# Kernel tuning notes

Hardware: AMD Instinct MI355X
Metric: run time of the kernel (lower is better)

The kernel has to match this reference:

```python
import jax, jax.numpy as jnp
import numpy as np

ATT_HEADS = 4
H_FEATS = 16
IN_FEATS = 64
N_NODES = 50000
N_EDGES = 1000000


def setup_inputs() -> dict:
    key = jax.random.key(0)
    ks = jax.random.split(key, 12)
    h = jax.random.normal(ks[0], (N_NODES, IN_FEATS), dtype=jnp.float32)
    src_idx = jax.random.randint(ks[1], (N_EDGES,), 0, N_NODES)
    dst_idx = jax.random.randint(ks[2], (N_EDGES,), 0, N_NODES)
    s = 1.0 / np.sqrt(IN_FEATS)
    # w_liner: Linear(in_feats, h_feats*att_heads)
    W_w = jax.random.uniform(ks[3], (IN_FEATS, H_FEATS * ATT_HEADS), jnp.float32, -s, s)
    b_w = jax.random.uniform(ks[4], (H_FEATS * ATT_HEADS,), jnp.float32, -s, s)
    # atten: Linear(2*h_feats, 1)
    sa = 1.0 / np.sqrt(2 * H_FEATS)
    W_a = jax.random.uniform(ks[5], (2 * H_FEATS, 1), jnp.float32, -sa, sa)
    b_a = jax.random.uniform(ks[6], (1,), jnp.float32, -sa, sa)
    # relation_aware: d_liner Linear(in_feats, in_feats), f_liner Linear(3*in_feats, 1)
    W_d = jax.random.uniform(ks[7], (IN_FEATS, IN_FEATS), jnp.float32, -s, s)
    b_d = jax.random.uniform(ks[8], (IN_FEATS,), jnp.float32, -s, s)
    sf = 1.0 / np.sqrt(3 * IN_FEATS)
    W_f = jax.random.uniform(ks[9], (3 * IN_FEATS, 1), jnp.float32, -sf, sf)
    b_f = jax.random.uniform(ks[10], (1,), jnp.float32, -sf, sf)
    return {"h": h, "src_idx": src_idx, "dst_idx": dst_idx,
            "W_w": W_w, "b_w": b_w, "W_a": W_a, "b_a": b_a,
            "W_d": W_d, "b_d": b_d, "W_f": W_f, "b_f": b_f}


def reference(h, src_idx, dst_idx, W_w, b_w, W_a, b_a, W_d, b_d, W_f, b_f):
    N = h.shape[0]
    # sign_edges: relation_aware score -> sign per edge
    s_feat = h[src_idx] @ W_d + b_d            # [E, F]
    d_feat = h[dst_idx] @ W_d + b_d            # [E, F]
    e_feat = jnp.concatenate([s_feat, d_feat, s_feat - d_feat], axis=-1)
    score = jnp.tanh(e_feat @ W_f + b_f)[:, 0]  # [E]
    sign = jnp.sign(score)
    # node transform
    hp = h @ W_w + b_w                          # [N, H*hf]
    # message: signed src features, per-head concat with dst, attention logit
    sf = (sign[:, None] * hp[src_idx]).reshape(-1, ATT_HEADS, H_FEATS)  # [E,H,hf]
    df = hp[dst_idx].reshape(-1, ATT_HEADS, H_FEATS)                    # [E,H,hf]
    z = jnp.concatenate([sf, df], axis=-1)                              # [E,H,2hf]
    alpha = jax.nn.leaky_relu(z @ W_a + b_a)                            # [E,H,1]
    # reduce: segment softmax over incoming edges of each dst node
    amax = jax.ops.segment_max(alpha, dst_idx, num_segments=N)          # [N,H,1]
    ex = jnp.exp(alpha - amax[dst_idx])
    esum = jax.ops.segment_sum(ex, dst_idx, num_segments=N)             # [N,H,1]
    w = ex / esum[dst_idx]                                              # [E,H,1]
    out = jax.ops.segment_sum(w * sf, dst_idx, num_segments=N)          # [N,H,hf]
    return out.reshape(N, ATT_HEADS * H_FEATS)
```

## Files before the change

### kernel.cpp

```cpp
#include <hip/hip_runtime.h>
#include <hip/hip_fp16.h>

constexpr int F  = 64;
constexpr int HEADS = 4;
constexpr int SHARDS = 8;
constexpr int CAPS = 16;
constexpr int MAXDEG = 64;

__global__ __launch_bounds__(256) void node_wd_kernel(
    const float* __restrict__ h,
    const float* __restrict__ W_d, const float* __restrict__ b_d,
    const float* __restrict__ W_f,
    float* __restrict__ tfeat,
    float* __restrict__ u_arr, float* __restrict__ v_arr,
    unsigned* __restrict__ cnt, unsigned* __restrict__ of_cnt, int N)
{
    __shared__ float sWT[F * F];
    __shared__ float sb[F];
    __shared__ double swfA[F], swfB[F];

    int tid = threadIdx.x;
    for (int i = tid; i < F * F; i += 256) {
        int k = i >> 6, j = i & 63;
        sWT[j * F + k] = W_d[i];
    }
    if (tid < F) {
        sb[tid] = b_d[tid];
        swfA[tid] = (double)W_f[tid] + (double)W_f[2 * F + tid];
        swfB[tid] = (double)W_f[F + tid] - (double)W_f[2 * F + tid];
    }
    if (blockIdx.x == 0 && tid == 0) *of_cnt = 0;
    __syncthreads();

    int n = blockIdx.x * 256 + tid;
    if (n >= N) return;

#pragma unroll
    for (int x = 0; x < SHARDS; x++) cnt[(size_t)x * N + n] = 0;

    float4 hv[16];
    const float4* h4 = reinterpret_cast<const float4*>(h + (size_t)n * F);
#pragma unroll
    for (int i = 0; i < 16; i++) hv[i] = h4[i];

    double u = 0.0, v = 0.0;
    float4 tq;
    float4* trow = reinterpret_cast<float4*>(tfeat + (size_t)n * F);
#pragma unroll 4
    for (int j = 0; j < F; j++) {
        const float4* row = reinterpret_cast<const float4*>(&sWT[j * F]);
        float t = 0.f;
#pragma unroll
        for (int kk = 0; kk < 16; kk++) {
            float4 w = row[kk];
            float4 x = hv[kk];
            t = fmaf(x.x, w.x, t);
            t = fmaf(x.y, w.y, t);
            t = fmaf(x.z, w.z, t);
            t = fmaf(x.w, w.w, t);
        }
        t = t + sb[j];
        u = fma((double)t, swfA[j], u);
        v = fma((double)t, swfB[j], v);
        if ((j & 3) == 0) tq.x = t;
        else if ((j & 3) == 1) tq.y = t;
        else if ((j & 3) == 2) tq.z = t;
        else { tq.w = t; trow[j >> 2] = tq; }
    }
    u_arr[n] = (float)u;
    v_arr[n] = (float)v;
}

__device__ __noinline__ float tier2_sign(
    const float* __restrict__ tfeat, const float* __restrict__ sWf,
    int s, int d, float bf)
{
    const float4* ts = reinterpret_cast<const float4*>(tfeat + (size_t)s * F);
    const float4* td = reinterpret_cast<const float4*>(tfeat + (size_t)d * F);
    float sv[F];
#pragma unroll
    for (int i = 0; i < 16; i++) {
        float4 a = ts[i];
        sv[4 * i + 0] = a.x; sv[4 * i + 1] = a.y;
        sv[4 * i + 2] = a.z; sv[4 * i + 3] = a.w;
    }
    float acc = 0.f;
#pragma unroll
    for (int j = 0; j < F; j++) acc = fmaf(sv[j], sWf[j], acc);
#pragma unroll
    for (int i = 0; i < 16; i++) {
        float4 a = td[i];
        acc = fmaf(a.x, sWf[F + 4 * i + 0], acc);
        acc = fmaf(a.y, sWf[F + 4 * i + 1], acc);
        acc = fmaf(a.z, sWf[F + 4 * i + 2], acc);
        acc = fmaf(a.w, sWf[F + 4 * i + 3], acc);
    }
#pragma unroll
    for (int i = 0; i < 16; i++) {
        float4 a = td[i];
        acc = fmaf(sv[4 * i + 0] - a.x, sWf[2 * F + 4 * i + 0], acc);
        acc = fmaf(sv[4 * i + 1] - a.y, sWf[2 * F + 4 * i + 1], acc);
        acc = fmaf(sv[4 * i + 2] - a.z, sWf[2 * F + 4 * i + 2], acc);
        acc = fmaf(sv[4 * i + 3] - a.w, sWf[2 * F + 4 * i + 3], acc);
    }
    float sp = acc + bf;
    return (sp > 0.f) ? 1.f : (sp < 0.f ? -1.f : 0.f);
}

__global__ __launch_bounds__(256) void ww_count_scatter_kernel(
    const float* __restrict__ h,
    const float* __restrict__ W_w, const float* __restrict__ b_w,
    const float* __restrict__ W_a,
    __half* __restrict__ hp,
    float* __restrict__ a_src, float* __restrict__ a_dst,
    const int* __restrict__ src_idx, const int* __restrict__ dst_idx,
    const float* __restrict__ u_arr, const float* __restrict__ v_arr,
    const float* __restrict__ tfeat, const float* __restrict__ W_f,
    const float* __restrict__ b_f,
    unsigned* __restrict__ cnt, unsigned* __restrict__ slot_src,
    unsigned char* __restrict__ sgn8,
    unsigned* __restrict__ of_list, unsigned* __restrict__ of_cnt,
    int N, int E, int nbw, unsigned of_cap)
{
    __shared__ float sWT[F * F];
    __shared__ float sb[F];
    __shared__ float sWa[32];

    int tid = threadIdx.x;

    if (blockIdx.x < nbw) {
        for (int i = tid; i < F * F; i += 256) {
            int k = i >> 6, j = i & 63;
            sWT[j * F + k] = W_w[i];
        }
        if (tid < F) sb[tid] = b_w[tid];
        if (tid < 32) sWa[tid] = W_a[tid];
        __syncthreads();

        int n = blockIdx.x * 256 + tid;
        if (n >= N) return;

        float4 hv[16];
        const float4* h4 = reinterpret_cast<const float4*>(h + (size_t)n * F);
#pragma unroll
        for (int i = 0; i < 16; i++) hv[i] = h4[i];

        __half2* prow = reinterpret_cast<__half2*>(hp + (size_t)n * F);
#pragma unroll
        for (int qh = 0; qh < 4; qh++) {
            float asq = 0.f, adq = 0.f;
            float pprev = 0.f;
#pragma unroll 4
            for (int jj = 0; jj < 16; jj++) {
                int j = qh * 16 + jj;
                const float4* row = reinterpret_cast<const float4*>(&sWT[j * F]);
                float p = 0.f;
#pragma unroll
                for (int kk = 0; kk < 16; kk++) {
                    float4 w = row[kk];
                    float4 x = hv[kk];
                    p = fmaf(x.x, w.x, p);
                    p = fmaf(x.y, w.y, p);
                    p = fmaf(x.z, w.z, p);
                    p = fmaf(x.w, w.w, p);
                }
                p = p + sb[j];
                asq = fmaf(p, sWa[jj], asq);
                adq = fmaf(p, sWa[16 + jj], adq);
                if ((jj & 1) == 0) pprev = p;
                else prow[j >> 1] = __floats2half2_rn(pprev, p);
            }
            a_src[n * HEADS + qh] = asq;
            a_dst[n * HEADS + qh] = adq;
        }
        return;
    }

    float* sWf = sWT;
    if (tid < 3 * F) sWf[tid] = W_f[tid];
    __syncthreads();

    unsigned xcc;
    asm volatile("s_getreg_b32 %0, hwreg(HW_REG_XCC_ID)" : "=s"(xcc));
    xcc &= (SHARDS - 1);

    float bf = b_f[0];
    int eb = blockIdx.x - nbw;
    int e0 = eb * 512 + tid;
    int e1 = e0 + 256;
    bool ok0 = e0 < E, ok1 = e1 < E;

    int s0 = 0, d0 = 0, s1 = 0, d1 = 0;
    if (ok0) { s0 = src_idx[e0]; d0 = dst_idx[e0]; }
    if (ok1) { s1 = src_idx[e1]; d1 = dst_idx[e1]; }

    float us0 = ok0 ? u_arr[s0] : 0.f, vd0 = ok0 ? v_arr[d0] : 0.f;
    float us1 = ok1 ? u_arr[s1] : 0.f, vd1 = ok1 ? v_arr[d1] : 0.f;
    unsigned p0 = ok0 ? __hip_atomic_fetch_add(&cnt[(size_t)xcc * N + d0], 1u,
                          __ATOMIC_RELAXED, __HIP_MEMORY_SCOPE_WORKGROUP) : 0u;
    unsigned p1 = ok1 ? __hip_atomic_fetch_add(&cnt[(size_t)xcc * N + d1], 1u,
                          __ATOMIC_RELAXED, __HIP_MEMORY_SCOPE_WORKGROUP) : 0u;

    bool inl0 = ok0 && (p0 < (unsigned)CAPS);
    bool inl1 = ok1 && (p1 < (unsigned)CAPS);
    size_t idx0 = ((size_t)xcc * N + d0) * CAPS + p0;
    size_t idx1 = ((size_t)xcc * N + d1) * CAPS + p1;
    if (inl0) slot_src[idx0] = (unsigned)s0;
    if (inl1) slot_src[idx1] = (unsigned)s1;

    float m0 = us0 + vd0 + bf;
    float m1 = us1 + vd1 + bf;
    float sg0 = (fabsf(m0) >= 1e-4f) ? ((m0 > 0.f) ? 1.f : -1.f)
              : (ok0 ? tier2_sign(tfeat, sWf, s0, d0, bf) : 0.f);
    float sg1 = (fabsf(m1) >= 1e-4f) ? ((m1 > 0.f) ? 1.f : -1.f)
              : (ok1 ? tier2_sign(tfeat, sWf, s1, d1, bf) : 0.f);
    unsigned c0 = (sg0 > 0.f) ? 0u : (sg0 < 0.f ? 1u : 2u);
    unsigned c1 = (sg1 > 0.f) ? 0u : (sg1 < 0.f ? 1u : 2u);

    if (inl0) sgn8[idx0] = (unsigned char)c0;
    else if (ok0) {
        unsigned oi = atomicAdd(of_cnt, 1u);
        if (oi < of_cap) { of_list[2 * oi] = (unsigned)d0; of_list[2 * oi + 1] = (unsigned)s0 | (c0 << 30); }
    }
    if (inl1) sgn8[idx1] = (unsigned char)c1;
    else if (ok1) {
        unsigned oi = atomicAdd(of_cnt, 1u);
        if (oi < of_cap) { of_list[2 * oi] = (unsigned)d1; of_list[2 * oi + 1] = (unsigned)s1 | (c1 << 30); }
    }
}

__global__ __launch_bounds__(256) void dst_gather_kernel(
    const unsigned* __restrict__ cnt,
    const unsigned* __restrict__ slot_src, const unsigned char* __restrict__ sgn8,
    const unsigned* __restrict__ of_list, const unsigned* __restrict__ of_cnt,
    const float* __restrict__ a_src, const float* __restrict__ a_dst,
    const float* __restrict__ b_a,
    const __half* __restrict__ hp,
    float* __restrict__ out, int N, unsigned of_cap)
{
    __shared__ float sw[4][MAXDEG * 4];
    __shared__ unsigned ssrc[4][MAXDEG];

    int tid = threadIdx.x;
    int wslot = tid >> 6;
    int lane = tid & 63;
    int q = lane >> 4;
    int d = (blockIdx.x * 256 + tid) >> 6;
    bool valid = d < N;

    float ba = b_a[0];
    float4 ad4 = make_float4(0.f, 0.f, 0.f, 0.f);
    unsigned csh[SHARDS], pre[SHARDS];
    unsigned deg = 0;
    bool ofl = false;
    if (valid) {
        ad4 = *reinterpret_cast<const float4*>(a_dst + (size_t)d * HEADS);
#pragma unroll
        for (int x = 0; x < SHARDS; x++) {
            unsigned c = cnt[(size_t)x * N + d];
            csh[x] = c; pre[x] = deg; deg += c;
            if (c > (unsigned)CAPS) ofl = true;
        }
    }
    float adq = (q == 0) ? ad4.x : (q == 1) ? ad4.y : (q == 2) ? ad4.z : ad4.w;
    bool fast = valid && (deg <= (unsigned)MAXDEG) && !ofl;

    float4 p = make_float4(0.f, 0.f, 0.f, 0.f);
    if (fast && lane < (int)deg) {
        int shard = 0; unsigned pos = 0;
#pragma unroll
        for (int x = 0; x < SHARDS; x++)
            if ((unsigned)lane >= pre[x] && (unsigned)lane < pre[x] + csh[x]) {
                shard = x; pos = (unsigned)lane - pre[x];
            }
        size_t idx = ((size_t)shard * N + d) * CAPS + pos;
        unsigned s = slot_src[idx];
        unsigned c = sgn8[idx];
        float sgn = (c == 0u) ? 1.f : (c == 1u ? -1.f : 0.f);
        float4 as4 = *reinterpret_cast<const float4*>(a_src + (size_t)s * HEADS);
        float ap0 = fmaf(sgn, as4.x, ad4.x) + ba;
        float ap1 = fmaf(sgn, as4.y, ad4.y) + ba;
        float ap2 = fmaf(sgn, as4.z, ad4.z) + ba;
        float ap3 = fmaf(sgn, as4.w, ad4.w) + ba;
        float e0 = expf(ap0 > 0.f ? ap0 : 0.01f * ap0);
        float e1 = expf(ap1 > 0.f ? ap1 : 0.01f * ap1);
        float e2 = expf(ap2 > 0.f ? ap2 : 0.01f * ap2);
        float e3 = expf(ap3 > 0.f ? ap3 : 0.01f * ap3);
        p = make_float4(e0, e1, e2, e3);
        *reinterpret_cast<float4*>(&sw[wslot][lane * 4]) =
            make_float4(sgn * e0, sgn * e1, sgn * e2, sgn * e3);
        ssrc[wslot][lane] = s;
    }
    if (valid && !fast) {
        for (int x = 0; x < SHARDS; x++) {
            unsigned cc = min(csh[x], (unsigned)CAPS);
            for (unsigned i = lane; i < cc; i += 64) {
                size_t idx = ((size_t)x * N + d) * CAPS + i;
                unsigned s = slot_src[idx];
                unsigned c = sgn8[idx];
                float sgn = (c == 0u) ? 1.f : (c == 1u ? -1.f : 0.f);
                float4 as4 = *reinterpret_cast<const float4*>(a_src + (size_t)s * HEADS);
                float ap0 = fmaf(sgn, as4.x, ad4.x) + ba;
                float ap1 = fmaf(sgn, as4.y, ad4.y) + ba;
                float ap2 = fmaf(sgn, as4.z, ad4.z) + ba;
                float ap3 = fmaf(sgn, as4.w, ad4.w) + ba;
                p.x += expf(ap0 > 0.f ? ap0 : 0.01f * ap0);
                p.y += expf(ap1 > 0.f ? ap1 : 0.01f * ap1);
                p.z += expf(ap2 > 0.f ? ap2 : 0.01f * ap2);
                p.w += expf(ap3 > 0.f ? ap3 : 0.01f * ap3);
            }
        }
        unsigned on = min(*of_cnt, of_cap);
        for (unsigned i = lane; i < on; i += 64) {
            if (of_list[2 * i] == (unsigned)d) {
                unsigned sp = of_list[2 * i + 1];
                unsigned s = sp & 0x3FFFFFFFu;
                unsigned c = sp >> 30;
                float sgn = (c == 0u) ? 1.f : (c == 1u ? -1.f : 0.f);
                float4 as4 = *reinterpret_cast<const float4*>(a_src + (size_t)s * HEADS);
                float ap0 = fmaf(sgn, as4.x, ad4.x) + ba;
                float ap1 = fmaf(sgn, as4.y, ad4.y) + ba;
                float ap2 = fmaf(sgn, as4.z, ad4.z) + ba;
                float ap3 = fmaf(sgn, as4.w, ad4.w) + ba;
                p.x += expf(ap0 > 0.f ? ap0 : 0.01f * ap0);
                p.y += expf(ap1 > 0.f ? ap1 : 0.01f * ap1);
                p.z += expf(ap2 > 0.f ? ap2 : 0.01f * ap2);
                p.w += expf(ap3 > 0.f ? ap3 : 0.01f * ap3);
            }
        }
    }
    __syncthreads();

#pragma unroll
    for (int off = 32; off >= 1; off >>= 1) {
        p.x += __shfl_xor(p.x, off);
        p.y += __shfl_xor(p.y, off);
        p.z += __shfl_xor(p.z, off);
        p.w += __shfl_xor(p.w, off);
    }
    if (!valid) return;

    float esq = (q == 0) ? p.x : (q == 1) ? p.y : (q == 2) ? p.z : p.w;
    float rinv = (deg > 0) ? (1.0f / esq) : 0.f;

    float a0 = 0.f, a1 = 0.f, a2 = 0.f, a3 = 0.f;
    if (fast) {
        const float* swb = &sw[wslot][0];
        const unsigned* ssb = &ssrc[wslot][0];
        unsigned t0 = 0;
        for (; t0 + 8 <= deg; t0 += 8) {
            float w0 = swb[(t0 + 0) * 4 + q], w1 = swb[(t0 + 1) * 4 + q];
            float w2 = swb[(t0 + 2) * 4 + q], w3 = swb[(t0 + 3) * 4 + q];
            float w4 = swb[(t0 + 4) * 4 + q], w5 = swb[(t0 + 5) * 4 + q];
            float w6 = swb[(t0 + 6) * 4 + q], w7 = swb[(t0 + 7) * 4 + q];
            unsigned s0 = ssb[t0 + 0], s1 = ssb[t0 + 1];
            unsigned s2 = ssb[t0 + 2], s3 = ssb[t0 + 3];
            unsigned s4 = ssb[t0 + 4], s5 = ssb[t0 + 5];
            unsigned s6 = ssb[t0 + 6], s7 = ssb[t0 + 7];
            float h0 = __half2float(hp[((size_t)s0 << 6) | (unsigned)lane]);
            float h1 = __half2float(hp[((size_t)s1 << 6) | (unsigned)lane]);
            float h2 = __half2float(hp[((size_t)s2 << 6) | (unsigned)lane]);
            float h3 = __half2float(hp[((size_t)s3 << 6) | (unsigned)lane]);
            float h4 = __half2float(hp[((size_t)s4 << 6) | (unsigned)lane]);
            float h5 = __half2float(hp[((size_t)s5 << 6) | (unsigned)lane]);
            float h6 = __half2float(hp[((size_t)s6 << 6) | (unsigned)lane]);
            float h7 = __half2float(hp[((size_t)s7 << 6) | (unsigned)lane]);
            a0 = fmaf(w0, h0, a0); a1 = fmaf(w1, h1, a1);
            a2 = fmaf(w2, h2, a2); a3 = fmaf(w3, h3, a3);
            a0 = fmaf(w4, h4, a0); a1 = fmaf(w5, h5, a1);
            a2 = fmaf(w6, h6, a2); a3 = fmaf(w7, h7, a3);
        }
        for (; t0 < deg; t0++) {
            float w = swb[t0 * 4 + q];
            unsigned s = ssb[t0];
            a0 = fmaf(w, __half2float(hp[((size_t)s << 6) | (unsigned)lane]), a0);
        }
    } else {
        for (int x = 0; x < SHARDS; x++) {
            unsigned cc = min(csh[x], (unsigned)CAPS);
            for (unsigned i = 0; i < cc; i++) {
                size_t idx = ((size_t)x * N + d) * CAPS + i;
                unsigned s = slot_src[idx];
                unsigned c = sgn8[idx];
                float g = (c == 0u) ? 1.f : (c == 1u ? -1.f : 0.f);
                float asv = a_src[s * HEADS + q];
                float ap = fmaf(g, asv, adq) + ba;
                float ev = expf(ap > 0.f ? ap : 0.01f * ap);
                a0 = fmaf(ev * g, __half2float(hp[((size_t)s << 6) | (unsigned)lane]), a0);
            }
        }
        unsigned on = min(*of_cnt, of_cap);
        for (unsigned i = 0; i < on; i++) {
            if (of_list[2 * i] == (unsigned)d) {
                unsigned sp = of_list[2 * i + 1];
                unsigned s = sp & 0x3FFFFFFFu;
                unsigned c = sp >> 30;
                float g = (c == 0u) ? 1.f : (c == 1u ? -1.f : 0.f);
                float asv = a_src[s * HEADS + q];
                float ap = fmaf(g, asv, adq) + ba;
                float ev = expf(ap > 0.f ? ap : 0.01f * ap);
                a0 = fmaf(ev * g, __half2float(hp[((size_t)s << 6) | (unsigned)lane]), a0);
            }
        }
    }
    out[((size_t)d << 6) | (unsigned)lane] = ((a0 + a1) + (a2 + a3)) * rinv;
}

extern "C" void kernel_launch(void* const* d_in, const int* in_sizes, int n_in,
                              void* d_out, int out_size, void* d_ws, size_t ws_size,
                              hipStream_t stream)
{
    const float* h       = (const float*)d_in[0];
    const int*   src_idx = (const int*)d_in[1];
    const int*   dst_idx = (const int*)d_in[2];
    const float* W_w     = (const float*)d_in[3];
    const float* b_w     = (const float*)d_in[4];
    const float* W_a     = (const float*)d_in[5];
    const float* b_a     = (const float*)d_in[6];
    const float* W_d     = (const float*)d_in[7];
    const float* b_d     = (const float*)d_in[8];
    const float* W_f     = (const float*)d_in[9];
    const float* b_f     = (const float*)d_in[10];

    int N = in_sizes[0] / F;
    int E = in_sizes[1];
    int nb = (N + 255) / 256;
    int neb = (E + 511) / 512;
    unsigned of_cap = (unsigned)(E / 8);

    char* ws = (char*)d_ws;
    float*         tfeat  = (float*)ws;         ws += (size_t)N * F * 4;
    __half*        hp     = (__half*)ws;        ws += (size_t)N * F * 2;
    float*         u_arr  = (float*)ws;         ws += (size_t)N * 4;
    float*         v_arr  = (float*)ws;         ws += (size_t)N * 4;
    float*         a_src  = (float*)ws;         ws += (size_t)N * HEADS * 4;
    float*         a_dst  = (float*)ws;         ws += (size_t)N * HEADS * 4;
    unsigned*      cnt    = (unsigned*)ws;      ws += (size_t)SHARDS * N * 4;
    unsigned*      of_cnt = (unsigned*)ws;      ws += 64;
    unsigned*      slot_s = (unsigned*)ws;      ws += (size_t)SHARDS * N * CAPS * 4;
    unsigned char* sgn8   = (unsigned char*)ws; ws += (size_t)SHARDS * N * CAPS;
    unsigned*      of_list= (unsigned*)ws;      ws += (size_t)of_cap * 8;

    float* out = (float*)d_out;

    node_wd_kernel<<<nb, 256, 0, stream>>>(
        h, W_d, b_d, W_f, tfeat, u_arr, v_arr, cnt, of_cnt, N);

    ww_count_scatter_kernel<<<nb + neb, 256, 0, stream>>>(
        h, W_w, b_w, W_a, hp, a_src, a_dst,
        src_idx, dst_idx, u_arr, v_arr, tfeat, W_f, b_f,
        cnt, slot_s, sgn8, of_list, of_cnt, N, E, nb, of_cap);

    dst_gather_kernel<<<(N * 64 + 255) / 256, 256, 0, stream>>>(
        cnt, slot_s, sgn8, of_list, of_cnt, a_src, a_dst, b_a, hp, out, N, of_cap);
}
```

Before: 128.0 us.

## Add per-node overflow bucket and halve per-shard slot capacity

```diff
diff --git a/kernel.cpp b/kernel.cpp
--- a/kernel.cpp
+++ b/kernel.cpp
@@ -4,7 +4,8 @@
 constexpr int F  = 64;
 constexpr int HEADS = 4;
 constexpr int SHARDS = 8;
-constexpr int CAPS = 16;
+constexpr int CAPS = 8;
+constexpr int OCAP = 56;
 constexpr int MAXDEG = 64;
 
 __global__ __launch_bounds__(256) void node_wd_kernel(
@@ -13,7 +14,8 @@
     const float* __restrict__ W_f,
     float* __restrict__ tfeat,
     float* __restrict__ u_arr, float* __restrict__ v_arr,
-    unsigned* __restrict__ cnt, unsigned* __restrict__ of_cnt, int N)
+    unsigned* __restrict__ cnt, unsigned* __restrict__ ocnt,
+    unsigned* __restrict__ of_cnt, int N)
 {
     __shared__ float sWT[F * F];
     __shared__ float sb[F];
@@ -37,6 +39,7 @@
 
 #pragma unroll
     for (int x = 0; x < SHARDS; x++) cnt[(size_t)x * N + n] = 0;
+    ocnt[n] = 0;
 
     float4 hv[16];
     const float4* h4 = reinterpret_cast<const float4*>(h + (size_t)n * F);
@@ -119,6 +122,7 @@
     const float* __restrict__ b_f,
     unsigned* __restrict__ cnt, unsigned* __restrict__ slot_src,
     unsigned char* __restrict__ sgn8,
+    unsigned* __restrict__ ocnt, unsigned* __restrict__ ovf,
     unsigned* __restrict__ of_list, unsigned* __restrict__ of_cnt,
     int N, int E, int nbw, unsigned of_cap)
 {
@@ -219,19 +223,28 @@
 
     if (inl0) sgn8[idx0] = (unsigned char)c0;
     else if (ok0) {
-        unsigned oi = atomicAdd(of_cnt, 1u);
-        if (oi < of_cap) { of_list[2 * oi] = (unsigned)d0; of_list[2 * oi + 1] = (unsigned)s0 | (c0 << 30); }
+        unsigned po = atomicAdd(&ocnt[d0], 1u);
+        if (po < (unsigned)OCAP) ovf[(size_t)d0 * OCAP + po] = (unsigned)s0 | (c0 << 30);
+        else {
+            unsigned oi = atomicAdd(of_cnt, 1u);
+            if (oi < of_cap) { of_list[2 * oi] = (unsigned)d0; of_list[2 * oi + 1] = (unsigned)s0 | (c0 << 30); }
+        }
     }
     if (inl1) sgn8[idx1] = (unsigned char)c1;
     else if (ok1) {
-        unsigned oi = atomicAdd(of_cnt, 1u);
-        if (oi < of_cap) { of_list[2 * oi] = (unsigned)d1; of_list[2 * oi + 1] = (unsigned)s1 | (c1 << 30); }
+        unsigned po = atomicAdd(&ocnt[d1], 1u);
+        if (po < (unsigned)OCAP) ovf[(size_t)d1 * OCAP + po] = (unsigned)s1 | (c1 << 30);
+        else {
+            unsigned oi = atomicAdd(of_cnt, 1u);
+            if (oi < of_cap) { of_list[2 * oi] = (unsigned)d1; of_list[2 * oi + 1] = (unsigned)s1 | (c1 << 30); }
+        }
     }
 }
 
 __global__ __launch_bounds__(256) void dst_gather_kernel(
     const unsigned* __restrict__ cnt,
     const unsigned* __restrict__ slot_src, const unsigned char* __restrict__ sgn8,
+    const unsigned* __restrict__ ocnt, const unsigned* __restrict__ ovf,
     const unsigned* __restrict__ of_list, const unsigned* __restrict__ of_cnt,
     const float* __restrict__ a_src, const float* __restrict__ a_dst,
     const float* __restrict__ b_a,
@@ -251,31 +264,41 @@
     float ba = b_a[0];
     float4 ad4 = make_float4(0.f, 0.f, 0.f, 0.f);
     unsigned csh[SHARDS], pre[SHARDS];
-    unsigned deg = 0;
-    bool ofl = false;
+    unsigned degS = 0, oc = 0, ocr = 0;
     if (valid) {
         ad4 = *reinterpret_cast<const float4*>(a_dst + (size_t)d * HEADS);
 #pragma unroll
         for (int x = 0; x < SHARDS; x++) {
             unsigned c = cnt[(size_t)x * N + d];
-            csh[x] = c; pre[x] = deg; deg += c;
-            if (c > (unsigned)CAPS) ofl = true;
-        }
+            csh[x] = min(c, (unsigned)CAPS);
+            pre[x] = degS;
+            degS += csh[x];
+        }
+        ocr = ocnt[d];
+        oc = min(ocr, (unsigned)OCAP);
     }
     float adq = (q == 0) ? ad4.x : (q == 1) ? ad4.y : (q == 2) ? ad4.z : ad4.w;
-    bool fast = valid && (deg <= (unsigned)MAXDEG) && !ofl;
+    unsigned degT = degS + oc;
+    bool fast = valid && (degT <= (unsigned)MAXDEG) && (ocr <= (unsigned)OCAP);
 
     float4 p = make_float4(0.f, 0.f, 0.f, 0.f);
-    if (fast && lane < (int)deg) {
-        int shard = 0; unsigned pos = 0;
-#pragma unroll
-        for (int x = 0; x < SHARDS; x++)
-            if ((unsigned)lane >= pre[x] && (unsigned)lane < pre[x] + csh[x]) {
-                shard = x; pos = (unsigned)lane - pre[x];
-            }
-        size_t idx = ((size_t)shard * N + d) * CAPS + pos;
-        unsigned s = slot_src[idx];
-        unsigned c = sgn8[idx];
+    if (fast && lane < (int)degT) {
+        unsigned s, c;
+        if ((unsigned)lane < degS) {
+            int shard = 0; unsigned pos = 0;
+#pragma unroll
+            for (int x = 0; x < SHARDS; x++)
+                if ((unsigned)lane >= pre[x] && (unsigned)lane < pre[x] + csh[x]) {
+                    shard = x; pos = (unsigned)lane - pre[x];
+                }
+            size_t idx = ((size_t)shard * N + d) * CAPS + pos;
+            s = slot_src[idx];
+            c = sgn8[idx];
+        } else {
+            unsigned v = ovf[(size_t)d * OCAP + ((unsigned)lane - degS)];
+            s = v & 0x3FFFFFFFu;
+            c = v >> 30;
+        }
         float sgn = (c == 0u) ? 1.f : (c == 1u ? -1.f : 0.f);
         float4 as4 = *reinterpret_cast<const float4*>(a_src + (size_t)s * HEADS);
         float ap0 = fmaf(sgn, as4.x, ad4.x) + ba;
@@ -293,8 +316,7 @@
     }
     if (valid && !fast) {
         for (int x = 0; x < SHARDS; x++) {
-            unsigned cc = min(csh[x], (unsigned)CAPS);
-            for (unsigned i = lane; i < cc; i += 64) {
+            for (unsigned i = lane; i < csh[x]; i += 64) {
                 size_t idx = ((size_t)x * N + d) * CAPS + i;
                 unsigned s = slot_src[idx];
                 unsigned c = sgn8[idx];
@@ -309,6 +331,21 @@
                 p.z += expf(ap2 > 0.f ? ap2 : 0.01f * ap2);
                 p.w += expf(ap3 > 0.f ? ap3 : 0.01f * ap3);
             }
+        }
+        for (unsigned i = lane; i < oc; i += 64) {
+            unsigned v = ovf[(size_t)d * OCAP + i];
+            unsigned s = v & 0x3FFFFFFFu;
+            unsigned c = v >> 30;
+            float sgn = (c == 0u) ? 1.f : (c == 1u ? -1.f : 0.f);
+            float4 as4 = *reinterpret_cast<const float4*>(a_src + (size_t)s * HEADS);
+            float ap0 = fmaf(sgn, as4.x, ad4.x) + ba;
+            float ap1 = fmaf(sgn, as4.y, ad4.y) + ba;
+            float ap2 = fmaf(sgn, as4.z, ad4.z) + ba;
+            float ap3 = fmaf(sgn, as4.w, ad4.w) + ba;
+            p.x += expf(ap0 > 0.f ? ap0 : 0.01f * ap0);
+            p.y += expf(ap1 > 0.f ? ap1 : 0.01f * ap1);
+            p.z += expf(ap2 > 0.f ? ap2 : 0.01f * ap2);
+            p.w += expf(ap3 > 0.f ? ap3 : 0.01f * ap3);
         }
         unsigned on = min(*of_cnt, of_cap);
         for (unsigned i = lane; i < on; i += 64) {
@@ -341,14 +378,14 @@
     if (!valid) return;
 
     float esq = (q == 0) ? p.x : (q == 1) ? p.y : (q == 2) ? p.z : p.w;
-    float rinv = (deg > 0) ? (1.0f / esq) : 0.f;
+    float rinv = (esq > 0.f) ? (1.0f / esq) : 0.f;
 
     float a0 = 0.f, a1 = 0.f, a2 = 0.f, a3 = 0.f;
     if (fast) {
         const float* swb = &sw[wslot][0];
         const unsigned* ssb = &ssrc[wslot][0];
         unsigned t0 = 0;
-        for (; t0 + 8 <= deg; t0 += 8) {
+        for (; t0 + 8 <= degT; t0 += 8) {
             float w0 = swb[(t0 + 0) * 4 + q], w1 = swb[(t0 + 1) * 4 + q];
             float w2 = swb[(t0 + 2) * 4 + q], w3 = swb[(t0 + 3) * 4 + q];
             float w4 = swb[(t0 + 4) * 4 + q], w5 = swb[(t0 + 5) * 4 + q];
@@ -370,15 +407,14 @@
             a0 = fmaf(w4, h4, a0); a1 = fmaf(w5, h5, a1);
             a2 = fmaf(w6, h6, a2); a3 = fmaf(w7, h7, a3);
         }
-        for (; t0 < deg; t0++) {
+        for (; t0 < degT; t0++) {
             float w = swb[t0 * 4 + q];
             unsigned s = ssb[t0];
             a0 = fmaf(w, __half2float(hp[((size_t)s << 6) | (unsigned)lane]), a0);
         }
     } else {
         for (int x = 0; x < SHARDS; x++) {
-            unsigned cc = min(csh[x], (unsigned)CAPS);
-            for (unsigned i = 0; i < cc; i++) {
+            for (unsigned i = 0; i < csh[x]; i++) {
                 size_t idx = ((size_t)x * N + d) * CAPS + i;
                 unsigned s = slot_src[idx];
                 unsigned c = sgn8[idx];
@@ -388,6 +424,16 @@
                 float ev = expf(ap > 0.f ? ap : 0.01f * ap);
                 a0 = fmaf(ev * g, __half2float(hp[((size_t)s << 6) | (unsigned)lane]), a0);
             }
+        }
+        for (unsigned i = 0; i < oc; i++) {
+            unsigned v = ovf[(size_t)d * OCAP + i];
+            unsigned s = v & 0x3FFFFFFFu;
+            unsigned c = v >> 30;
+            float g = (c == 0u) ? 1.f : (c == 1u ? -1.f : 0.f);
+            float asv = a_src[s * HEADS + q];
+            float ap = fmaf(g, asv, adq) + ba;
+            float ev = expf(ap > 0.f ? ap : 0.01f * ap);
+            a0 = fmaf(ev * g, __half2float(hp[((size_t)s << 6) | (unsigned)lane]), a0);
         }
         unsigned on = min(*of_cnt, of_cap);
         for (unsigned i = 0; i < on; i++) {
@@ -426,7 +472,7 @@
     int E = in_sizes[1];
     int nb = (N + 255) / 256;
     int neb = (E + 511) / 512;
-    unsigned of_cap = (unsigned)(E / 8);
+    unsigned of_cap = (unsigned)(E / 16);
 
     char* ws = (char*)d_ws;
     float*         tfeat  = (float*)ws;         ws += (size_t)N * F * 4;
@@ -436,21 +482,24 @@
     float*         a_src  = (float*)ws;         ws += (size_t)N * HEADS * 4;
     float*         a_dst  = (float*)ws;         ws += (size_t)N * HEADS * 4;
     unsigned*      cnt    = (unsigned*)ws;      ws += (size_t)SHARDS * N * 4;
+    unsigned*      ocnt   = (unsigned*)ws;      ws += (size_t)N * 4;
     unsigned*      of_cnt = (unsigned*)ws;      ws += 64;
     unsigned*      slot_s = (unsigned*)ws;      ws += (size_t)SHARDS * N * CAPS * 4;
     unsigned char* sgn8   = (unsigned char*)ws; ws += (size_t)SHARDS * N * CAPS;
+    unsigned*      ovf    = (unsigned*)ws;      ws += (size_t)N * OCAP * 4;
     unsigned*      of_list= (unsigned*)ws;      ws += (size_t)of_cap * 8;
 
     float* out = (float*)d_out;
 
     node_wd_kernel<<<nb, 256, 0, stream>>>(
-        h, W_d, b_d, W_f, tfeat, u_arr, v_arr, cnt, of_cnt, N);
+        h, W_d, b_d, W_f, tfeat, u_arr, v_arr, cnt, ocnt, of_cnt, N);
 
     ww_count_scatter_kernel<<<nb + neb, 256, 0, stream>>>(
         h, W_w, b_w, W_a, hp, a_src, a_dst,
         src_idx, dst_idx, u_arr, v_arr, tfeat, W_f, b_f,
-        cnt, slot_s, sgn8, of_list, of_cnt, N, E, nb, of_cap);
+        cnt, slot_s, sgn8, ocnt, ovf, of_list, of_cnt, N, E, nb, of_cap);
 
     dst_gather_kernel<<<(N * 64 + 255) / 256, 256, 0, stream>>>(
-        cnt, slot_s, sgn8, of_list, of_cnt, a_src, a_dst, b_a, hp, out, N, of_cap);
+        cnt, slot_s, sgn8, ocnt, ovf, of_list, of_cnt,
+        a_src, a_dst, b_a, hp, out, N, of_cap);
 }
```

Measured after the change: 123.1 us. 3.9% less time.
